# Performance work log

Measured on AMD Instinct MI355X. Metric: run time of the kernel, lower is better.

The kernel has to match this reference:

```python
import jax, jax.numpy as jnp
import numpy as np

S, D, H, FF = 2048, 1024, 16, 4096
DH = D // H
EPS = 1e-5


def gelu(x):
    return 0.5 * x * (1 + jnp.tanh(jnp.sqrt(2 / jnp.pi) * (x + 0.044715 * jnp.power(x, 3))))


def layer_norm(x, w, b):
    mu = jnp.mean(x, axis=-1, keepdims=True)
    var = jnp.mean(jnp.square(x - mu), axis=-1, keepdims=True)
    return (x - mu) * jnp.power(var + EPS, -0.5) * w + b


def glorot(key, shape):
    fan_in, fan_out = shape[0], shape[1]
    lim = jnp.sqrt(6.0 / (fan_in + fan_out))
    return jax.random.uniform(key, shape, jnp.float32, -lim, lim)


def setup_inputs() -> dict:
    key = jax.random.key(0)
    ks = jax.random.split(key, 6)
    return {
        "x": jax.random.normal(ks[0], (S, D), jnp.float32),
        "W_qkv": glorot(ks[1], (D, 3 * D)),
        "W_o": glorot(ks[2], (D, D)),
        "W1": glorot(ks[3], (D, FF)),
        "b1": jnp.zeros((FF,), jnp.float32),
        "W2": glorot(ks[4], (FF, D)),
        "b2": jnp.zeros((D,), jnp.float32),
        "ln_att_w": jnp.ones((D,), jnp.float32),
        "ln_att_b": jnp.zeros((D,), jnp.float32),
        "ln_mlp_w": jnp.ones((D,), jnp.float32),
        "ln_mlp_b": jnp.zeros((D,), jnp.float32),
    }


def attention(x, W_qkv, W_o):
    qkv = (x @ W_qkv).reshape(S, 3, H, DH)
    q, k, v = qkv[:, 0], qkv[:, 1], qkv[:, 2]  # each [S, H, DH]
    # scores [H, S_q, S_k]
    scores = jnp.einsum("qhd,khd->hqk", q, k) / jnp.sqrt(jnp.float32(DH))
    causal = jnp.tril(jnp.ones((S, S), bool))
    scores = jnp.where(causal[None], scores, -jnp.inf)
    w = jax.nn.softmax(scores, axis=2)
    out = jnp.einsum("hqk,khd->qhd", w, v).reshape(S, D)
    return out @ W_o


def reference(x, W_qkv, W_o, W1, b1, W2, b2, ln_att_w, ln_att_b, ln_mlp_w, ln_mlp_b):
    x = x + attention(layer_norm(x, ln_att_w, ln_att_b), W_qkv, W_o)
    h = layer_norm(x, ln_mlp_w, ln_mlp_b)
    mlp_out = gelu(h @ W1 + b1) @ W2 + b2
    return x + mlp_out
```

## Files before the change

### kernel.cpp

```cpp
#include <hip/hip_runtime.h>
#include <math.h>

typedef __bf16 bf16;
typedef __bf16 bf16x4 __attribute__((ext_vector_type(4)));
typedef __bf16 bf16x8 __attribute__((ext_vector_type(8)));
typedef float f32x4 __attribute__((ext_vector_type(4)));
typedef unsigned short u16;
typedef unsigned short u16x8 __attribute__((ext_vector_type(8)));
typedef unsigned int u32;

__device__ __forceinline__ u16 f2bf(float f) {
  union { float f; u32 u; } v; v.f = f;
  u32 u = v.u;
  return (u16)((u + 0x7FFFu + ((u >> 16) & 1u)) >> 16);
}
__device__ __forceinline__ float bf2f(u16 u) {
  union { u32 u; float f; } v; v.u = (u32)u << 16;
  return v.f;
}

__device__ __forceinline__ f32x4 mfma16(bf16x8 a, bf16x8 b, f32x4 c) {
  return __builtin_amdgcn_mfma_f32_16x16x32_bf16(a, b, c, 0, 0, 0);
}

__device__ __forceinline__ size_t pk_addr(int r, int c, int C) {
  return ((size_t)(r >> 4) * (C >> 5) + (c >> 5)) * 512 +
         ((c >> 3) & 3) * 128 + (r & 15) * 8 + (c & 7);
}

__device__ __forceinline__ void wconv_body(const float* __restrict__ W,
                                           u16* __restrict__ Wt, int K, int N,
                                           int bx, int by) {
  __shared__ float tile[64][65];
  const int k0 = by * 64, n0 = bx * 64;
  const int t = threadIdx.x;
  const int tr = t >> 4;
  const int tc = (t & 15) * 4;
#pragma unroll
  for (int it = 0; it < 4; it++) {
    const int r = tr + it * 16;
    const float4 v = *(const float4*)(W + (size_t)(k0 + r) * N + n0 + tc);
    tile[r][tc] = v.x; tile[r][tc + 1] = v.y; tile[r][tc + 2] = v.z; tile[r][tc + 3] = v.w;
  }
  __syncthreads();
#pragma unroll
  for (int it = 0; it < 4; it++) {
    const int rn = tr + it * 16;
    const int n = n0 + rn;
    const int k = k0 + tc;
    ushort4 o;
    o.x = f2bf(tile[tc][rn]);
    o.y = f2bf(tile[tc + 1][rn]);
    o.z = f2bf(tile[tc + 2][rn]);
    o.w = f2bf(tile[tc + 3][rn]);
    *(ushort4*)(Wt + pk_addr(n, k, K)) = o;
  }
}

__device__ __forceinline__ void ln_body(const float* __restrict__ x,
                                        const float* __restrict__ w,
                                        const float* __restrict__ b,
                                        u16* __restrict__ out, int row) {
  const int t = threadIdx.x;
  const float4 v = *(const float4*)(x + (size_t)row * 1024 + t * 4);
  float s = v.x + v.y + v.z + v.w;
  float s2 = v.x * v.x + v.y * v.y + v.z * v.z + v.w * v.w;
#pragma unroll
  for (int m = 1; m < 64; m <<= 1) {
    s += __shfl_xor(s, m);
    s2 += __shfl_xor(s2, m);
  }
  __shared__ float red[8];
  if ((t & 63) == 0) { red[t >> 6] = s; red[4 + (t >> 6)] = s2; }
  __syncthreads();
  s = red[0] + red[1] + red[2] + red[3];
  s2 = red[4] + red[5] + red[6] + red[7];
  const float mu = s * (1.f / 1024.f);
  const float var = fmaxf(s2 * (1.f / 1024.f) - mu * mu, 0.f);
  const float rstd = rsqrtf(var + 1e-5f);
  const float* wp = w + t * 4;
  const float* bp = b + t * 4;
  ushort4 o;
  o.x = f2bf((v.x - mu) * rstd * wp[0] + bp[0]);
  o.y = f2bf((v.y - mu) * rstd * wp[1] + bp[1]);
  o.z = f2bf((v.z - mu) * rstd * wp[2] + bp[2]);
  o.w = f2bf((v.w - mu) * rstd * wp[3] + bp[3]);
  *(ushort4*)(out + pk_addr(row, t * 4, 1024)) = o;
}

__global__ __launch_bounds__(256)
void prep_all(const float* __restrict__ Wqkv, const float* __restrict__ Wo,
              const float* __restrict__ W1, const float* __restrict__ W2,
              const float* __restrict__ x, const float* __restrict__ ln_aw,
              const float* __restrict__ ln_ab,
              u16* __restrict__ Wqkv_t, u16* __restrict__ Wo_t,
              u16* __restrict__ W1_t, u16* __restrict__ W2_t,
              u16* __restrict__ h1) {
  const int id = blockIdx.x;
  if (id < 768)       { wconv_body(Wqkv, Wqkv_t, 1024, 3072, id % 48, id / 48); }
  else if (id < 1024) { const int j = id - 768;  wconv_body(Wo, Wo_t, 1024, 1024, j % 16, j / 16); }
  else if (id < 2048) { const int j = id - 1024; wconv_body(W1, W1_t, 1024, 4096, j % 64, j / 64); }
  else if (id < 3072) { const int j = id - 2048; wconv_body(W2, W2_t, 4096, 1024, j % 16, j / 16); }
  else                { ln_body(x, ln_aw, ln_ab, h1, id - 3072); }
}

__global__ __launch_bounds__(256)
void reduce_ln(const float* __restrict__ x, const u16* __restrict__ pb,
               const float* __restrict__ w, const float* __restrict__ b,
               float* __restrict__ x2, u16* __restrict__ h2) {
  const int row = blockIdx.x;
  const int t = threadIdx.x;
  const size_t base = (size_t)row * 1024 + t * 4;
  float4 v = *(const float4*)(x + base);
#pragma unroll
  for (int z = 0; z < 4; z++) {
    const ushort4 p = *(const ushort4*)(pb + (size_t)z * 2097152 + base);
    v.x += bf2f(p.x); v.y += bf2f(p.y); v.z += bf2f(p.z); v.w += bf2f(p.w);
  }
  *(float4*)(x2 + base) = v;
  float s = v.x + v.y + v.z + v.w;
  float s2 = v.x * v.x + v.y * v.y + v.z * v.z + v.w * v.w;
#pragma unroll
  for (int m = 1; m < 64; m <<= 1) {
    s += __shfl_xor(s, m);
    s2 += __shfl_xor(s2, m);
  }
  __shared__ float red[8];
  if ((t & 63) == 0) { red[t >> 6] = s; red[4 + (t >> 6)] = s2; }
  __syncthreads();
  s = red[0] + red[1] + red[2] + red[3];
  s2 = red[4] + red[5] + red[6] + red[7];
  const float mu = s * (1.f / 1024.f);
  const float var = fmaxf(s2 * (1.f / 1024.f) - mu * mu, 0.f);
  const float rstd = rsqrtf(var + 1e-5f);
  const float* wp = w + t * 4;
  const float* bp = b + t * 4;
  ushort4 o;
  o.x = f2bf((v.x - mu) * rstd * wp[0] + bp[0]);
  o.y = f2bf((v.y - mu) * rstd * wp[1] + bp[1]);
  o.z = f2bf((v.z - mu) * rstd * wp[2] + bp[2]);
  o.w = f2bf((v.w - mu) * rstd * wp[3] + bp[3]);
  *(ushort4*)(h2 + pk_addr(row, t * 4, 1024)) = o;
}

__global__ __launch_bounds__(256)
void reduce_out(const float* __restrict__ x2, const float* __restrict__ bias,
                const u16* __restrict__ pb, float* __restrict__ out) {
  const size_t base = ((size_t)blockIdx.x * 256 + threadIdx.x) * 4;
  const int col = (int)(base & 1023);
  float4 v = *(const float4*)(x2 + base);
  const float4 bb = *(const float4*)(bias + col);
  v.x += bb.x; v.y += bb.y; v.z += bb.z; v.w += bb.w;
#pragma unroll
  for (int z = 0; z < 4; z++) {
    const ushort4 p = *(const ushort4*)(pb + (size_t)z * 2097152 + base);
    v.x += bf2f(p.x); v.y += bf2f(p.y); v.z += bf2f(p.z); v.w += bf2f(p.w);
  }
  *(float4*)(out + base) = v;
}

template <int EPI, int KS>
__global__ __launch_bounds__(256, 3)
void gemm_pk(const u16* __restrict__ Ap, const u16* __restrict__ Bp,
             int M, int N, int K,
             const float* __restrict__ bias, u16* __restrict__ pb,
             u16* __restrict__ outB,
             u16* __restrict__ qo, u16* __restrict__ ko, u16* __restrict__ vo) {
  const int t = threadIdx.x;
  const int l = t & 63;
  const int w = t >> 6;
  const int WR = (w >> 1) * 64, WC = (w & 1) * 64;
  const int l15 = l & 15, lg = l >> 4;

  const int nx = gridDim.x;
  const u32 bid = blockIdx.y * nx + blockIdx.x;
  const int nxc = nx >> 3;
  const u32 r = bid >> 3;
  const int bx = (bid & 7) * nxc + (int)(r % (u32)nxc);
  const int by = (int)(r / (u32)nxc);

  const int m0 = by * 128, n0 = bx * 128;
  const int KT = K >> 5;
  const int nt = (K / KS) >> 5;
  const int t0 = blockIdx.z * nt;

  const u16* aB = Ap + ((size_t)((m0 + WR) >> 4) * KT + t0) * 512 + l * 8;
  const u16* bB = Bp + ((size_t)((n0 + WC) >> 4) * KT + t0) * 512 + l * 8;

  f32x4 acc[4][4] = {};
  bf16x8 a0[4], b0[4], a1[4], b1[4];

  auto LD = [&](bf16x8 (&af)[4], bf16x8 (&bf_)[4], int ti) {
#pragma unroll
    for (int i = 0; i < 4; i++)
      af[i] = *(const bf16x8*)(aB + ((size_t)i * KT + ti) * 512);
#pragma unroll
    for (int j = 0; j < 4; j++)
      bf_[j] = *(const bf16x8*)(bB + ((size_t)j * KT + ti) * 512);
  };
  auto FMA = [&](bf16x8 (&af)[4], bf16x8 (&bf_)[4]) {
    __builtin_amdgcn_s_setprio(1);
#pragma unroll
    for (int i = 0; i < 4; i++)
#pragma unroll
      for (int j = 0; j < 4; j++)
        acc[i][j] = mfma16(af[i], bf_[j], acc[i][j]);
    __builtin_amdgcn_s_setprio(0);
  };

  LD(a0, b0, 0);
  for (int ti = 0; ti < nt; ti += 2) {
    LD(a1, b1, (ti + 1 < nt) ? ti + 1 : ti);
    FMA(a0, b0);
    LD(a0, b0, (ti + 2 < nt) ? ti + 2 : ti);
    FMA(a1, b1);
  }

  const int mr0 = m0 + WR + lg * 4;
  const int nc0 = n0 + WC + l15;
#pragma unroll
  for (int i = 0; i < 4; i++) {
    const int mr = mr0 + i * 16;
#pragma unroll
    for (int j = 0; j < 4; j++) {
      const int nc = nc0 + j * 16;
      if (EPI == 0) {
        const int sel = nc >> 10;
        const int d = nc & 1023;
        const int h = d >> 6, dl = d & 63;
        const int kt2 = mr >> 5;
        if (sel == 2) {
          const int lgp = (mr >> 3) & 3, el0 = mr & 7;
          const int nb = dl >> 4, l15p = dl & 15;
          u16* dst = vo + (size_t)(h * 64 + kt2) * 2048 + nb * 512 +
                     (lgp * 16 + l15p) * 8 + el0;
          ushort4 o;
          o.x = f2bf(acc[i][j][0]); o.y = f2bf(acc[i][j][1]);
          o.z = f2bf(acc[i][j][2]); o.w = f2bf(acc[i][j][3]);
          *(ushort4*)dst = o;
        } else {
          const int f = (mr >> 4) & 1, l15p0 = mr & 15;
          const int kk = dl >> 5, lgp = (dl >> 3) & 3, el = dl & 7;
          u16* dst = (sel == 0 ? qo : ko) + (size_t)(h * 64 + kt2) * 2048 +
                     f * 1024 + kk * 512 + (lgp * 16 + l15p0) * 8 + el;
#pragma unroll
          for (int e = 0; e < 4; e++)
            dst[e * 8] = f2bf(acc[i][j][e]);
        }
      } else if (EPI == 2) {
        const float bb = bias[nc];
#pragma unroll
        for (int e = 0; e < 4; e++) {
          const float v = acc[i][j][e] + bb;
          const float g = 0.5f * v * (1.0f + tanhf(0.7978845608028654f * (v + 0.044715f * v * v * v)));
          outB[pk_addr(mr + e, nc, 4096)] = f2bf(g);
        }
      } else {
        u16* po = pb + (size_t)blockIdx.z * M * N;
#pragma unroll
        for (int e = 0; e < 4; e++)
          po[(size_t)(mr + e) * N + nc] = f2bf(acc[i][j][e]);
      }
    }
  }
}

__device__ __forceinline__ void attn_load(
    bf16x8 (&kf)[2][2], bf16x8 (&vf)[4],
    const u16* __restrict__ Kp, const u16* __restrict__ Vp,
    int hkt, int l) {
#pragma unroll
  for (int f = 0; f < 2; f++)
#pragma unroll
    for (int kk = 0; kk < 2; kk++)
      kf[kk][f] = *(const bf16x8*)(Kp + hkt + f * 1024 + kk * 512 + l * 8);
#pragma unroll
  for (int nb = 0; nb < 4; nb++)
    vf[nb] = *(const bf16x8*)(Vp + hkt + nb * 512 + l * 8);
}

__device__ __forceinline__ void attn_tile(
    const bf16x8 (&kf)[2][2], const bf16x8 (&vf)[4], const bf16x8 (&qf)[2][2],
    f32x4 (&accO)[2][4], float (&lsum)[2], u16* myP,
    int k0, bool diag, int qb, int l15, int lg) {
  f32x4 sv[2][2] = {};
  __builtin_amdgcn_s_setprio(1);
#pragma unroll
  for (int g = 0; g < 2; g++)
#pragma unroll
    for (int f = 0; f < 2; f++)
#pragma unroll
      for (int kk = 0; kk < 2; kk++)
        sv[g][f] = mfma16(kf[kk][f], qf[g][kk], sv[g][f]);
  __builtin_amdgcn_s_setprio(0);
#pragma unroll
  for (int g = 0; g < 2; g++) {
#pragma unroll
    for (int f = 0; f < 2; f++) {
      bf16x4 pk;
      float ps = 0.f;
#pragma unroll
      for (int e = 0; e < 4; e++) {
        float p = exp2f(sv[g][f][e] * 0.1803368801f);
        if (diag && (k0 + f * 16 + lg * 4 + e > qb + g * 16 + l15)) p = 0.f;
        ps += p;
        pk[e] = (bf16)p;
      }
      lsum[g] += ps;
      *(bf16x4*)(myP + g * 640 + l15 * 40 + f * 16 + lg * 4) = pk;
    }
  }
  const bf16x8 pf0 = *(const bf16x8*)(myP + l15 * 40 + lg * 8);
  const bf16x8 pf1 = *(const bf16x8*)(myP + 640 + l15 * 40 + lg * 8);
  __builtin_amdgcn_s_setprio(1);
#pragma unroll
  for (int nb = 0; nb < 4; nb++) {
    accO[0][nb] = mfma16(pf0, vf[nb], accO[0][nb]);
    accO[1][nb] = mfma16(pf1, vf[nb], accO[1][nb]);
  }
  __builtin_amdgcn_s_setprio(0);
}

__global__ __launch_bounds__(256)
void attn_fwd(const u16* __restrict__ Qp, const u16* __restrict__ Kp,
              const u16* __restrict__ Vp, u16* __restrict__ Ob) {
  __shared__ __attribute__((aligned(16))) char smem[33280];
  float* sO = (float*)smem;
  float* sL = (float*)(smem + 32768);
  u16* lP = (u16*)smem;

  const int t = threadIdx.x;
  const int l = t & 63, w = t >> 6;
  const int l15 = l & 15, lg = l >> 4;
  const u32 bid = blockIdx.x;
  const u32 vb = (bid & 7) * 128 + (bid >> 3);
  const int h = (int)(vb >> 6);
  const int qt = 63 - (int)(vb & 63);
  const int qb = qt * 32;

  u16* myPA = lP + w * 1280;
  u16* myPB = lP + 5120 + w * 1280;

  bf16x8 qf[2][2];
#pragma unroll
  for (int g = 0; g < 2; g++)
#pragma unroll
    for (int kk = 0; kk < 2; kk++)
      qf[g][kk] = *(const bf16x8*)(Qp + (size_t)(h * 64 + qt) * 2048 +
                                   g * 1024 + kk * 512 + l * 8);

  f32x4 accO[2][4] = {};
  float lsum[2] = {0.f, 0.f};

  if (w <= qt) {
    const int hb = h * 64;
    bf16x8 kfA[2][2], vfA[4], kfB[2][2], vfB[4];
    attn_load(kfA, vfA, Kp, Vp, (hb + w) * 2048, l);
    int kt = w;
    while (true) {
      const int ktB = kt + 4;
      const bool hasB = (ktB <= qt);
      attn_load(kfB, vfB, Kp, Vp, (hb + (hasB ? ktB : kt)) * 2048, l);
      attn_tile(kfA, vfA, qf, accO, lsum, myPA, kt * 32, kt == qt, qb, l15, lg);
      if (!hasB) break;
      const int ktA = kt + 8;
      const bool hasA = (ktA <= qt);
      attn_load(kfA, vfA, Kp, Vp, (hb + (hasA ? ktA : ktB)) * 2048, l);
      attn_tile(kfB, vfB, qf, accO, lsum, myPB, ktB * 32, ktB == qt, qb, l15, lg);
      if (!hasA) break;
      kt = ktA;
    }
  }

  float lsr[2];
#pragma unroll
  for (int g = 0; g < 2; g++) {
    float v = lsum[g];
    v += __shfl_xor(v, 16);
    v += __shfl_xor(v, 32);
    lsr[g] = v;
  }

  __syncthreads();
#pragma unroll
  for (int g = 0; g < 2; g++) {
#pragma unroll
    for (int nb = 0; nb < 4; nb++)
#pragma unroll
      for (int e = 0; e < 4; e++)
        sO[w * 2048 + (g * 16 + lg * 4 + e) * 64 + nb * 16 + l15] = accO[g][nb][e];
    if (lg == 0) sL[w * 32 + g * 16 + l15] = lsr[g];
  }
  __syncthreads();

  const int base = t * 8;
  const int row = base >> 6;
  const int col = base & 63;
  f32x4 a0 = {}, a1 = {};
  float ls = 0.f;
#pragma unroll
  for (int ww = 0; ww < 4; ww++) {
    a0 += *(const f32x4*)&sO[ww * 2048 + base];
    a1 += *(const f32x4*)&sO[ww * 2048 + base + 4];
    ls += sL[ww * 32 + row];
  }
  const float rinv = 1.0f / ls;
  u16x8 o;
#pragma unroll
  for (int j = 0; j < 4; j++) {
    o[j] = f2bf(a0[j] * rinv);
    o[4 + j] = f2bf(a1[j] * rinv);
  }
  const int grow = qb + row;
  const int gcol = h * 64 + col;
  *(u16x8*)(Ob + pk_addr(grow, gcol, 1024)) = o;
}

extern "C" void kernel_launch(void* const* d_in, const int* in_sizes, int n_in,
                              void* d_out, int out_size, void* d_ws, size_t ws_size,
                              hipStream_t stream) {
  const float* x     = (const float*)d_in[0];
  const float* W_qkv = (const float*)d_in[1];
  const float* W_o   = (const float*)d_in[2];
  const float* W1    = (const float*)d_in[3];
  const float* b1    = (const float*)d_in[4];
  const float* W2    = (const float*)d_in[5];
  const float* b2    = (const float*)d_in[6];
  const float* ln_aw = (const float*)d_in[7];
  const float* ln_ab = (const float*)d_in[8];
  const float* ln_mw = (const float*)d_in[9];
  const float* ln_mb = (const float*)d_in[10];

  char* ws = (char*)d_ws;
  u16* Wqkv_t = (u16*)(ws);
  u16* Wo_t   = (u16*)(ws + 6291456);
  u16* W1_t   = (u16*)(ws + 8388608);
  u16* W2_t   = (u16*)(ws + 16777216);
  u16* h1     = (u16*)(ws + 25165824);
  u16* h2     = h1;
  u16* Qp     = (u16*)(ws + 29360128);
  u16* Kp     = (u16*)(ws + 33554432);
  u16* Vp     = (u16*)(ws + 37748736);
  u16* attnb  = (u16*)(ws + 41943040);
  u16* ffb    = (u16*)(ws + 29360128);
  u16* pb     = (u16*)(ws + 46137344);
  float* x2   = (float*)(ws + 62914560);
  (void)ws_size; (void)in_sizes; (void)n_in; (void)out_size;

  prep_all<<<5120, 256, 0, stream>>>(W_qkv, W_o, W1, W2, x, ln_aw, ln_ab,
                                     Wqkv_t, Wo_t, W1_t, W2_t, h1);

  gemm_pk<0, 1><<<dim3(24, 16), 256, 0, stream>>>(
      h1, Wqkv_t, 2048, 3072, 1024, nullptr, nullptr, nullptr, Qp, Kp, Vp);

  attn_fwd<<<1024, 256, 0, stream>>>(Qp, Kp, Vp, attnb);

  gemm_pk<4, 4><<<dim3(8, 16, 4), 256, 0, stream>>>(
      attnb, Wo_t, 2048, 1024, 1024, nullptr, pb, nullptr, nullptr, nullptr, nullptr);

  reduce_ln<<<2048, 256, 0, stream>>>(x, pb, ln_mw, ln_mb, x2, h2);

  gemm_pk<2, 1><<<dim3(32, 16), 256, 0, stream>>>(
      h2, W1_t, 2048, 4096, 1024, b1, nullptr, ffb, nullptr, nullptr, nullptr);

  gemm_pk<4, 4><<<dim3(8, 16, 4), 256, 0, stream>>>(
      ffb, W2_t, 2048, 1024, 4096, nullptr, pb, nullptr, nullptr, nullptr, nullptr);

  reduce_out<<<2048, 256, 0, stream>>>(x2, b2, pb, (float*)d_out);
}
```

Measured before the change: 151.6 us.

## Double attention query tile to 64 rows per block to reuse K/V loads

The attention kernel now processes 64 query rows per block instead of 32, so each K/V tile loaded into registers feeds twice as many MFMAs. The grid is halved to 512 blocks and the block-to-(head, q-tile) mapping, the causal diagonal handling and the LDS reduction buffers are enlarged to match. This cuts total K/V global traffic and per-tile load overhead. In exchange it raises register pressure, doubles shared memory, and leaves fewer blocks for load balancing across CUs.

```diff
diff --git a/kernel.cpp b/kernel.cpp
--- a/kernel.cpp
+++ b/kernel.cpp
@@ -280,13 +280,13 @@
 }
 
 __device__ __forceinline__ void attn_tile(
-    const bf16x8 (&kf)[2][2], const bf16x8 (&vf)[4], const bf16x8 (&qf)[2][2],
-    f32x4 (&accO)[2][4], float (&lsum)[2], u16* myP,
+    const bf16x8 (&kf)[2][2], const bf16x8 (&vf)[4], const bf16x8 (&qf)[4][2],
+    f32x4 (&accO)[4][4], float (&lsum)[4], u16* myP,
     int k0, bool diag, int qb, int l15, int lg) {
-  f32x4 sv[2][2] = {};
+  f32x4 sv[4][2] = {};
   __builtin_amdgcn_s_setprio(1);
 #pragma unroll
-  for (int g = 0; g < 2; g++)
+  for (int g = 0; g < 4; g++)
 #pragma unroll
     for (int f = 0; f < 2; f++)
 #pragma unroll
@@ -294,7 +294,7 @@
         sv[g][f] = mfma16(kf[kk][f], qf[g][kk], sv[g][f]);
   __builtin_amdgcn_s_setprio(0);
 #pragma unroll
-  for (int g = 0; g < 2; g++) {
+  for (int g = 0; g < 4; g++) {
 #pragma unroll
     for (int f = 0; f < 2; f++) {
       bf16x4 pk;
@@ -310,71 +310,75 @@
       *(bf16x4*)(myP + g * 640 + l15 * 40 + f * 16 + lg * 4) = pk;
     }
   }
-  const bf16x8 pf0 = *(const bf16x8*)(myP + l15 * 40 + lg * 8);
-  const bf16x8 pf1 = *(const bf16x8*)(myP + 640 + l15 * 40 + lg * 8);
+  bf16x8 pf[4];
+#pragma unroll
+  for (int g = 0; g < 4; g++)
+    pf[g] = *(const bf16x8*)(myP + g * 640 + l15 * 40 + lg * 8);
   __builtin_amdgcn_s_setprio(1);
 #pragma unroll
-  for (int nb = 0; nb < 4; nb++) {
-    accO[0][nb] = mfma16(pf0, vf[nb], accO[0][nb]);
-    accO[1][nb] = mfma16(pf1, vf[nb], accO[1][nb]);
-  }
+  for (int nb = 0; nb < 4; nb++)
+#pragma unroll
+    for (int g = 0; g < 4; g++)
+      accO[g][nb] = mfma16(pf[g], vf[nb], accO[g][nb]);
   __builtin_amdgcn_s_setprio(0);
 }
 
 __global__ __launch_bounds__(256)
 void attn_fwd(const u16* __restrict__ Qp, const u16* __restrict__ Kp,
               const u16* __restrict__ Vp, u16* __restrict__ Ob) {
-  __shared__ __attribute__((aligned(16))) char smem[33280];
+  __shared__ __attribute__((aligned(16))) char smem[66560];
   float* sO = (float*)smem;
-  float* sL = (float*)(smem + 32768);
+  float* sL = (float*)(smem + 65536);
   u16* lP = (u16*)smem;
 
   const int t = threadIdx.x;
   const int l = t & 63, w = t >> 6;
   const int l15 = l & 15, lg = l >> 4;
   const u32 bid = blockIdx.x;
-  const u32 vb = (bid & 7) * 128 + (bid >> 3);
-  const int h = (int)(vb >> 6);
-  const int qt = 63 - (int)(vb & 63);
-  const int qb = qt * 32;
-
-  u16* myPA = lP + w * 1280;
-  u16* myPB = lP + 5120 + w * 1280;
-
-  bf16x8 qf[2][2];
-#pragma unroll
-  for (int g = 0; g < 2; g++)
+  const u32 vb = (bid & 7) * 64 + (bid >> 3);
+  const int h = (int)(vb >> 5);
+  const int qt = 31 - (int)(vb & 31);
+  const int qb = qt * 64;
+  const int nk = 2 * qt + 2;
+  const int dg0 = 2 * qt;
+
+  u16* myPA = lP + w * 2560;
+  u16* myPB = lP + 10240 + w * 2560;
+
+  bf16x8 qf[4][2];
+#pragma unroll
+  for (int g = 0; g < 4; g++)
 #pragma unroll
     for (int kk = 0; kk < 2; kk++)
-      qf[g][kk] = *(const bf16x8*)(Qp + (size_t)(h * 64 + qt) * 2048 +
-                                   g * 1024 + kk * 512 + l * 8);
-
-  f32x4 accO[2][4] = {};
-  float lsum[2] = {0.f, 0.f};
-
-  if (w <= qt) {
+      qf[g][kk] = *(const bf16x8*)(Qp + (size_t)(h * 64 + 2 * qt + (g >> 1)) * 2048 +
+                                   (g & 1) * 1024 + kk * 512 + l * 8);
+
+  f32x4 accO[4][4] = {};
+  float lsum[4] = {0.f, 0.f, 0.f, 0.f};
+
+  if (w < nk) {
     const int hb = h * 64;
     bf16x8 kfA[2][2], vfA[4], kfB[2][2], vfB[4];
     attn_load(kfA, vfA, Kp, Vp, (hb + w) * 2048, l);
     int kt = w;
     while (true) {
       const int ktB = kt + 4;
-      const bool hasB = (ktB <= qt);
+      const bool hasB = (ktB < nk);
       attn_load(kfB, vfB, Kp, Vp, (hb + (hasB ? ktB : kt)) * 2048, l);
-      attn_tile(kfA, vfA, qf, accO, lsum, myPA, kt * 32, kt == qt, qb, l15, lg);
+      attn_tile(kfA, vfA, qf, accO, lsum, myPA, kt * 32, kt >= dg0, qb, l15, lg);
       if (!hasB) break;
       const int ktA = kt + 8;
-      const bool hasA = (ktA <= qt);
+      const bool hasA = (ktA < nk);
       attn_load(kfA, vfA, Kp, Vp, (hb + (hasA ? ktA : ktB)) * 2048, l);
-      attn_tile(kfB, vfB, qf, accO, lsum, myPB, ktB * 32, ktB == qt, qb, l15, lg);
+      attn_tile(kfB, vfB, qf, accO, lsum, myPB, ktB * 32, ktB >= dg0, qb, l15, lg);
       if (!hasA) break;
       kt = ktA;
     }
   }
 
-  float lsr[2];
-#pragma unroll
-  for (int g = 0; g < 2; g++) {
+  float lsr[4];
+#pragma unroll
+  for (int g = 0; g < 4; g++) {
     float v = lsum[g];
     v += __shfl_xor(v, 16);
     v += __shfl_xor(v, 32);
@@ -383,37 +387,42 @@
 
   __syncthreads();
 #pragma unroll
-  for (int g = 0; g < 2; g++) {
+  for (int g = 0; g < 4; g++) {
 #pragma unroll
     for (int nb = 0; nb < 4; nb++)
 #pragma unroll
       for (int e = 0; e < 4; e++)
-        sO[w * 2048 + (g * 16 + lg * 4 + e) * 64 + nb * 16 + l15] = accO[g][nb][e];
-    if (lg == 0) sL[w * 32 + g * 16 + l15] = lsr[g];
+        sO[w * 4096 + (g * 16 + lg * 4 + e) * 64 + nb * 16 + l15] = accO[g][nb][e];
+    if (lg == 0) sL[w * 64 + g * 16 + l15] = lsr[g];
   }
   __syncthreads();
 
-  const int base = t * 8;
-  const int row = base >> 6;
-  const int col = base & 63;
-  f32x4 a0 = {}, a1 = {};
+  const int row = t >> 2;
+  const int c0 = (t & 3) * 16;
+  f32x4 a0 = {}, a1 = {}, a2 = {}, a3 = {};
   float ls = 0.f;
 #pragma unroll
   for (int ww = 0; ww < 4; ww++) {
-    a0 += *(const f32x4*)&sO[ww * 2048 + base];
-    a1 += *(const f32x4*)&sO[ww * 2048 + base + 4];
-    ls += sL[ww * 32 + row];
+    const float* p = &sO[ww * 4096 + row * 64 + c0];
+    a0 += *(const f32x4*)(p);
+    a1 += *(const f32x4*)(p + 4);
+    a2 += *(const f32x4*)(p + 8);
+    a3 += *(const f32x4*)(p + 12);
+    ls += sL[ww * 64 + row];
   }
   const float rinv = 1.0f / ls;
-  u16x8 o;
+  u16x8 o0, o1;
 #pragma unroll
   for (int j = 0; j < 4; j++) {
-    o[j] = f2bf(a0[j] * rinv);
-    o[4 + j] = f2bf(a1[j] * rinv);
+    o0[j] = f2bf(a0[j] * rinv);
+    o0[4 + j] = f2bf(a1[j] * rinv);
+    o1[j] = f2bf(a2[j] * rinv);
+    o1[4 + j] = f2bf(a3[j] * rinv);
   }
   const int grow = qb + row;
-  const int gcol = h * 64 + col;
-  *(u16x8*)(Ob + pk_addr(grow, gcol, 1024)) = o;
+  const int gcol = h * 64 + c0;
+  *(u16x8*)(Ob + pk_addr(grow, gcol, 1024)) = o0;
+  *(u16x8*)(Ob + pk_addr(grow, gcol + 8, 1024)) = o1;
 }
 
 extern "C" void kernel_launch(void* const* d_in, const int* in_sizes, int n_in,
@@ -453,7 +462,7 @@
   gemm_pk<0, 1><<<dim3(24, 16), 256, 0, stream>>>(
       h1, Wqkv_t, 2048, 3072, 1024, nullptr, nullptr, nullptr, Qp, Kp, Vp);
 
-  attn_fwd<<<1024, 256, 0, stream>>>(Qp, Kp, Vp, attnb);
+  attn_fwd<<<512, 256, 0, stream>>>(Qp, Kp, Vp, attnb);
 
   gemm_pk<4, 4><<<dim3(8, 16, 4), 256, 0, stream>>>(
       attnb, Wo_t, 2048, 1024, 1024, nullptr, pb, nullptr, nullptr, nullptr, nullptr);
```

After: 158.8 us. 1.05x slower.
